# Optimization experiments

Hardware: AMD Instinct MI355X
Metric: run time of the kernel (lower is better)

The kernel has to match this reference:

```python
import jax, jax.numpy as jnp
import numpy as np

SHIFTS = 1
WINDOW_SIZES = (4, 8, 16)
BN_EPS = 1e-5


def _calc_attn_path(x, ws, shifts):
    # x: (b, H, W, 2c) with channels laid out as (qv=2, c)
    b, H, W, c2 = x.shape
    c = c2 // 2
    if shifts > 0:
        x = jnp.roll(x, shift=(-ws // 2, -ws // 2), axis=(1, 2))
    h, w = H // ws, W // ws
    # 'b (h dh) (w dw) (qv c) -> qv (b h w) (dh dw c)'
    qv = x.reshape(b, h, ws, w, ws, 2, c).transpose(5, 0, 1, 3, 2, 4, 6)
    qv = qv.reshape(2, b * h * w, ws * ws * c)
    q, v = qv[0], qv[1]                       # (N, D), N = b*h*w windows, D = ws*ws*c
    atn = jax.nn.softmax(q @ q.T, axis=-1)    # (N, N) attention across windows (as in source)
    y = atn @ v                               # (N, D)
    # '(b h w) (dh dw c) -> b (h dh) (w dw) c'
    y = y.reshape(b, h, w, ws, ws, c).transpose(0, 1, 3, 2, 4, 5).reshape(b, H, W, c)
    if shifts > 0:
        y = jnp.roll(y, shift=(ws // 2, ws // 2), axis=(1, 2))
    return y, atn


def setup_inputs() -> dict:
    key = jax.random.key(0)
    ks = jax.random.split(key, 3)
    B, H, W, C = 4, 128, 128, 180
    inputs = jax.random.normal(ks[0], (B, H, W, C), jnp.float32)
    conv1_w = jax.random.normal(ks[1], (1, 1, C, 2 * C), jnp.float32) * 0.05
    conv1_b = jnp.zeros((2 * C,), jnp.float32)
    bn_scale = jnp.ones((2 * C,), jnp.float32)
    bn_bias = jnp.zeros((2 * C,), jnp.float32)
    conv2_w = jax.random.normal(ks[2], (1, 1, C, C), jnp.float32) * 0.05
    conv2_b = jnp.zeros((C,), jnp.float32)
    return {"inputs": inputs, "conv1_w": conv1_w, "conv1_b": conv1_b,
            "bn_scale": bn_scale, "bn_bias": bn_bias,
            "conv2_w": conv2_w, "conv2_b": conv2_b}


def reference(inputs, conv1_w, conv1_b, bn_scale, bn_bias, conv2_w, conv2_b):
    # 1x1 conv to 2*C channels (calc_attn=True)
    x = jnp.einsum('bhwc,cd->bhwd', inputs, conv1_w[0, 0]) + conv1_b
    # BatchNorm in training mode (batch statistics)
    mean = x.mean(axis=(0, 1, 2))
    var = x.var(axis=(0, 1, 2))
    x = (x - mean) * jax.lax.rsqrt(var + BN_EPS) * bn_scale + bn_bias
    xs = jnp.split(x, 3, axis=-1)             # three groups of 2*C/3 channels
    ys, attns = [], []
    for ws, xi in zip(WINDOW_SIZES, xs):
        y, a = _calc_attn_path(xi, ws, SHIFTS)
        ys.append(y)
        attns.append(a)
    y = jnp.concatenate(ys, axis=-1)          # back to C channels
    y = jnp.einsum('bhwc,cd->bhwd', y, conv2_w[0, 0]) + conv2_b
    return (y, *attns)
```

## Files before the change

### kernel.cpp

```cpp
#include <hip/hip_runtime.h>

typedef unsigned short u16;
typedef __bf16 bf16x8 __attribute__((ext_vector_type(8)));
typedef float f32x4 __attribute__((ext_vector_type(4)));
typedef u16 u16x4 __attribute__((ext_vector_type(4)));
typedef u16 u16x8 __attribute__((ext_vector_type(8)));

__device__ __forceinline__ u16 f2bf(float v) {
    unsigned u = __float_as_uint(v);
    unsigned r = (u + 0x7fffu + ((u >> 16) & 1u)) >> 16;
    return (u16)r;
}
__device__ __forceinline__ float bf2f(u16 u) { return __uint_as_float(((unsigned)u) << 16); }

__device__ __forceinline__ void async_cp16(const u16* g, u16* l) {
    __builtin_amdgcn_global_load_lds((const __attribute__((address_space(1))) unsigned int*)g,
                                     (__attribute__((address_space(3))) unsigned int*)l, 16, 0, 0);
}

__device__ __forceinline__ int xcd_swz(int local, int n) {
    const int q = n >> 3, r = n & 7;
    const int xcd = local & 7, j = local >> 3;
    const int base = xcd < r ? xcd * (q + 1) : r * (q + 1) + (xcd - r) * q;
    return base + j;
}

#define LKSWZ(tid) ((((tid) & 3) ^ (((tid) >> 3) & 3)) << 3)
#define ROSWZ(lane) (((lane) & 15) * 32 + ((((lane) >> 4) ^ (((lane) >> 1) & 3)) << 3))

__global__ __launch_bounds__(256) void gemm_f32(
    const u16* __restrict__ A, const u16* __restrict__ B,
    float* __restrict__ C, const float* __restrict__ bias,
    int K, int ldc, int n_store)
{
    __shared__ char smem[32768];
    u16* As = (u16*)smem;
    u16* Bs = (u16*)(smem + 8192);
    const int tid = threadIdx.x;
    const int lane = tid & 63;
    const int wave = tid >> 6;
    const int wm = wave >> 1, wn = wave & 1;
    const long m0 = (long)blockIdx.y * 128;
    const long n0 = (long)blockIdx.x * 128;

    f32x4 acc[4][4] = {};
    const int lrow = tid >> 2;
    const int lk = LKSWZ(tid);
    const u16* Ag = A + (m0 + lrow) * (long)K + lk;
    const u16* Bg = B + (n0 + lrow) * (long)K + lk;
    u16* Asl = As + tid * 8;
    u16* Bsl = Bs + tid * 8;
    const long K64 = (long)64 * K;
    const int ro = ROSWZ(lane);
    const int nsteps = K >> 5;

    async_cp16(Ag, Asl);
    async_cp16(Ag + K64, Asl + 2048);
    async_cp16(Bg, Bsl);
    async_cp16(Bg + K64, Bsl + 2048);
    __syncthreads();

    int cur = 0;
    for (int s = 0; s < nsteps; s++) {
        if (s + 1 < nsteps) {
            const int kn = (s + 1) << 5;
            u16* An = Asl + ((cur ^ 1) << 13);
            u16* Bn = Bsl + ((cur ^ 1) << 13);
            async_cp16(Ag + kn, An);
            async_cp16(Ag + kn + K64, An + 2048);
            async_cp16(Bg + kn, Bn);
            async_cp16(Bg + kn + K64, Bn + 2048);
        }
        bf16x8 af[4], bg[4];
        const u16* Asc = As + (cur << 13);
        const u16* Bsc = Bs + (cur << 13);
#pragma unroll
        for (int i = 0; i < 4; i++) af[i] = *(const bf16x8*)(Asc + (wm * 64 + i * 16) * 32 + ro);
#pragma unroll
        for (int j = 0; j < 4; j++) bg[j] = *(const bf16x8*)(Bsc + (wn * 64 + j * 16) * 32 + ro);
#pragma unroll
        for (int i = 0; i < 4; i++)
#pragma unroll
            for (int j = 0; j < 4; j++)
                acc[i][j] = __builtin_amdgcn_mfma_f32_16x16x32_bf16(af[i], bg[j], acc[i][j], 0, 0, 0);
        __syncthreads();
        cur ^= 1;
    }

    float bv[4];
#pragma unroll
    for (int j = 0; j < 4; j++) bv[j] = bias[n0 + wn * 64 + j * 16 + (lane & 15)];

    float* Cs = (float*)smem;
    for (int c = 0; c < 4; c++) {
        __syncthreads();
        if (wm == (c >> 1)) {
#pragma unroll
            for (int ii = 0; ii < 2; ii++) {
                const int i = (c & 1) * 2 + ii;
#pragma unroll
                for (int j = 0; j < 4; j++)
#pragma unroll
                    for (int r = 0; r < 4; r++) {
                        const int lr = ii * 16 + ((lane >> 4) << 2) + r;
                        Cs[lr * 128 + wn * 64 + j * 16 + (lane & 15)] = acc[i][j][r] + bv[j];
                    }
            }
        }
        __syncthreads();
        const int lr = tid >> 3;
        const int cg = (tid & 7) * 16;
        const long rowg = m0 + c * 32 + lr;
#pragma unroll
        for (int e = 0; e < 4; e++) {
            const int colg = cg + e * 4;
            if ((int)n0 + colg < n_store)
                *(f32x4*)(C + rowg * (long)ldc + n0 + colg) = *(const f32x4*)(Cs + lr * 128 + colg);
        }
    }
}

__global__ __launch_bounds__(256) void conv1_gemm(
    const float* __restrict__ A, const u16* __restrict__ B,
    u16* __restrict__ C, const float* __restrict__ bias)
{
    __shared__ char smem[16384];
    u16* As = (u16*)smem;
    u16* Bs = (u16*)(smem + 8192);
    const int tid = threadIdx.x;
    const int lane = tid & 63;
    const int wave = tid >> 6;
    const int wm = wave >> 1, wn = wave & 1;
    const long m0 = (long)blockIdx.y * 128;
    const long n0 = (long)blockIdx.x * 128;

    f32x4 acc[4][4] = {};
    const int lrow = tid >> 2;
    const int lk = LKSWZ(tid);
    const float* Ar0 = A + (m0 + lrow) * 180L;
    const float* Ar1 = Ar0 + 64 * 180L;
    const u16* Bg = B + (n0 + lrow) * 192L + lk;
    u16* Asl = As + tid * 8;
    u16* Bsl = Bs + tid * 8;
    const int ro = ROSWZ(lane);

#pragma unroll
    for (int k0 = 0; k0 < 192; k0 += 32) {
        const int gk = k0 + lk;
        u16x8 oa, ob;
        if (gk + 8 <= 180) {
            f32x4 a0 = *(const f32x4*)(Ar0 + gk), a1 = *(const f32x4*)(Ar0 + gk + 4);
            f32x4 b0 = *(const f32x4*)(Ar1 + gk), b1 = *(const f32x4*)(Ar1 + gk + 4);
#pragma unroll
            for (int c = 0; c < 4; c++) {
                oa[c] = f2bf(a0[c]); oa[4 + c] = f2bf(a1[c]);
                ob[c] = f2bf(b0[c]); ob[4 + c] = f2bf(b1[c]);
            }
        } else if (gk < 180) {
            f32x4 a0 = *(const f32x4*)(Ar0 + gk);
            f32x4 b0 = *(const f32x4*)(Ar1 + gk);
#pragma unroll
            for (int c = 0; c < 4; c++) {
                oa[c] = f2bf(a0[c]); oa[4 + c] = 0;
                ob[c] = f2bf(b0[c]); ob[4 + c] = 0;
            }
        } else {
#pragma unroll
            for (int c = 0; c < 8; c++) { oa[c] = 0; ob[c] = 0; }
        }
        *(u16x8*)Asl = oa;
        *(u16x8*)(Asl + 2048) = ob;
        async_cp16(Bg + k0, Bsl);
        async_cp16(Bg + k0 + 64 * 192, Bsl + 2048);
        __syncthreads();
        bf16x8 af[4], bg[4];
#pragma unroll
        for (int i = 0; i < 4; i++) af[i] = *(const bf16x8*)(As + (wm * 64 + i * 16) * 32 + ro);
#pragma unroll
        for (int j = 0; j < 4; j++) bg[j] = *(const bf16x8*)(Bs + (wn * 64 + j * 16) * 32 + ro);
#pragma unroll
        for (int i = 0; i < 4; i++)
#pragma unroll
            for (int j = 0; j < 4; j++)
                acc[i][j] = __builtin_amdgcn_mfma_f32_16x16x32_bf16(af[i], bg[j], acc[i][j], 0, 0, 0);
        __syncthreads();
    }

    float bv[4];
#pragma unroll
    for (int j = 0; j < 4; j++) bv[j] = bias[n0 + wn * 64 + j * 16 + (lane & 15)];

    u16* Cs = (u16*)smem;
    for (int c = 0; c < 2; c++) {
        __syncthreads();
        if (wm == c) {
#pragma unroll
            for (int i = 0; i < 4; i++)
#pragma unroll
                for (int j = 0; j < 4; j++)
#pragma unroll
                    for (int r = 0; r < 4; r++) {
                        const int lr = i * 16 + ((lane >> 4) << 2) + r;
                        Cs[lr * 128 + wn * 64 + j * 16 + (lane & 15)] = f2bf(acc[i][j][r] + bv[j]);
                    }
        }
        __syncthreads();
        const int lr = tid >> 2;
        const int cg = (tid & 3) * 32;
        const long rowg = m0 + c * 64 + lr;
#pragma unroll
        for (int e = 0; e < 4; e++) {
            const int colg = cg + e * 8;
            *(u16x8*)(C + rowg * 384L + n0 + colg) = *(const u16x8*)(Cs + lr * 128 + colg);
        }
    }
}

#define KLOOP_3BUF(Asv, Bsv, Aslv, Bslv, AgV, BgV, kbegV, K64V, nstepsV, roV)                 \
    {                                                                                          \
        async_cp16(AgV + kbegV, Aslv);                                                         \
        async_cp16(AgV + kbegV + K64V, Aslv + 2048);                                           \
        async_cp16(BgV + kbegV, Bslv);                                                         \
        async_cp16(BgV + kbegV + K64V, Bslv + 2048);                                           \
        if (nstepsV > 1) {                                                                     \
            const int kn = kbegV + 32;                                                         \
            async_cp16(AgV + kn, Aslv + 8192);                                                 \
            async_cp16(AgV + kn + K64V, Aslv + 8192 + 2048);                                   \
            async_cp16(BgV + kn, Bslv + 8192);                                                 \
            async_cp16(BgV + kn + K64V, Bslv + 8192 + 2048);                                   \
        }                                                                                      \
        int rb = 0, wb = 2;                                                                    \
        for (int s = 0; s < nstepsV; s++) {                                                    \
            if (s + 1 < nstepsV) { asm volatile("s_waitcnt vmcnt(4)" ::: "memory"); }          \
            else                 { asm volatile("s_waitcnt vmcnt(0)" ::: "memory"); }          \
            __builtin_amdgcn_sched_barrier(0);                                                 \
            __builtin_amdgcn_s_barrier();                                                      \
            __builtin_amdgcn_sched_barrier(0);                                                 \
            if (s + 2 < nstepsV) {                                                             \
                const int kn = kbegV + ((s + 2) << 5);                                         \
                u16* An = Aslv + wb * 8192;                                                    \
                u16* Bn = Bslv + wb * 8192;                                                    \
                async_cp16(AgV + kn, An);                                                      \
                async_cp16(AgV + kn + K64V, An + 2048);                                        \
                async_cp16(BgV + kn, Bn);                                                      \
                async_cp16(BgV + kn + K64V, Bn + 2048);                                        \
            }                                                                                  \
            bf16x8 af[4], bgf[4];                                                              \
            const u16* Asc = Asv + rb * 8192;                                                  \
            const u16* Bsc = Bsv + rb * 8192;                                                  \
            _Pragma("unroll")                                                                  \
            for (int i = 0; i < 4; i++) af[i] = *(const bf16x8*)(Asc + (wm * 64 + i * 16) * 32 + roV); \
            _Pragma("unroll")                                                                  \
            for (int j = 0; j < 4; j++) bgf[j] = *(const bf16x8*)(Bsc + (wn * 64 + j * 16) * 32 + roV); \
            _Pragma("unroll")                                                                  \
            for (int i = 0; i < 4; i++)                                                        \
                _Pragma("unroll")                                                              \
                for (int j = 0; j < 4; j++)                                                    \
                    acc[i][j] = __builtin_amdgcn_mfma_f32_16x16x32_bf16(af[i], bgf[j], acc[i][j], 0, 0, 0); \
            rb = rb == 2 ? 0 : rb + 1;                                                         \
            wb = wb == 2 ? 0 : wb + 1;                                                         \
        }                                                                                      \
    }

__global__ __launch_bounds__(256, 3) void qq_all(
    const u16* __restrict__ q0, const u16* __restrict__ q1, const u16* __restrict__ q2,
    float* __restrict__ S0, float* __restrict__ pG1, float* __restrict__ pG2)
{
    __shared__ char smem[49152];
    u16* As = (u16*)smem;
    u16* Bs = (u16*)(smem + 8192);
    const int bid = blockIdx.x;
    int seg, local;
    if (bid < 528) { seg = 0; local = xcd_swz(bid, 528); }
    else if (bid < 816) { seg = 1; local = xcd_swz(bid - 528, 288); }
    else { seg = 2; local = xcd_swz(bid - 816, 180); }
    const int tX = seg == 0 ? 32 : (seg == 1 ? 8 : 2);
    const int TT = (tX * (tX + 1)) >> 1;
    const int K = seg == 0 ? 1024 : (seg == 1 ? 3840 : 15360);
    const int Ksplit = seg == 0 ? 1024 : (seg == 1 ? 480 : 256);
    const int N = seg == 0 ? 4096 : (seg == 1 ? 1024 : 256);
    const u16* A = seg == 0 ? q0 : (seg == 1 ? q1 : q2);
    float* outP = seg == 0 ? S0 : (seg == 1 ? pG1 : pG2);
    const int z = local / TT;
    int rem = local - z * TT;
    int by = 0, rowlen = tX;
    while (rem >= rowlen) { rem -= rowlen; by++; rowlen--; }
    const int bx = by + rem;

    const int tid = threadIdx.x;
    const int lane = tid & 63;
    const int wave = tid >> 6;
    const int wm = wave >> 1, wn = wave & 1;
    const long m0 = (long)by * 128;
    const long n0 = (long)bx * 128;
    const int kbeg = z * Ksplit;

    f32x4 acc[4][4] = {};
    const int lrow = tid >> 2;
    const int lk = LKSWZ(tid);
    const u16* Ag = A + (m0 + lrow) * (long)K + lk;
    const u16* Bg = A + (n0 + lrow) * (long)K + lk;
    u16* Asl = As + tid * 8;
    u16* Bsl = Bs + tid * 8;
    const long K64 = (long)64 * K;
    const int ro = ROSWZ(lane);
    const int nsteps = Ksplit >> 5;

    KLOOP_3BUF(As, Bs, Asl, Bsl, Ag, Bg, kbeg, K64, nsteps, ro);

    float* Pz = outP + (long)z * N * N;

    if (bx != by) {
        const int r0 = (int)n0 + wn * 64 + (lane & 15);
        const int c0 = (int)m0 + wm * 64 + ((lane >> 4) << 2);
#pragma unroll
        for (int j = 0; j < 4; j++) {
            float* rp = Pz + (long)(r0 + j * 16) * N + c0;
#pragma unroll
            for (int i = 0; i < 4; i++)
                *(f32x4*)(rp + i * 16) = acc[i][j];
        }
    }

    float* Cs = (float*)smem;
    for (int c = 0; c < 4; c++) {
        __syncthreads();
        if (wm == (c >> 1)) {
#pragma unroll
            for (int ii = 0; ii < 2; ii++) {
                const int i = (c & 1) * 2 + ii;
#pragma unroll
                for (int j = 0; j < 4; j++)
#pragma unroll
                    for (int r = 0; r < 4; r++) {
                        const int lr = ii * 16 + ((lane >> 4) << 2) + r;
                        Cs[lr * 128 + wn * 64 + j * 16 + (lane & 15)] = acc[i][j][r];
                    }
            }
        }
        __syncthreads();
        const int lr = tid >> 3;
        const int cg = (tid & 7) * 16;
        const long rowg = m0 + c * 32 + lr;
#pragma unroll
        for (int e = 0; e < 4; e++) {
            const int colg = cg + e * 4;
            *(f32x4*)(Pz + rowg * (long)N + n0 + colg) = *(const f32x4*)(Cs + lr * 128 + colg);
        }
    }
}

__global__ __launch_bounds__(256, 3) void pv_all(
    const u16* __restrict__ a0, const u16* __restrict__ a1, const u16* __restrict__ a2,
    const u16* __restrict__ vt0, const u16* __restrict__ vt1, const u16* __restrict__ vt2,
    u16* __restrict__ Ysp, float* __restrict__ pP0, float* __restrict__ pP1)
{
    __shared__ char smem[49152];
    u16* As = (u16*)smem;
    u16* Bs = (u16*)(smem + 8192);
    const int bid = blockIdx.x;
    int seg, local, z = 0;
    if (bid < 512) { seg = 0; const int l = xcd_swz(bid, 512); z = l >> 8; local = l & 255; }
    else if (bid < 752) { seg = 1; local = xcd_swz(bid - 512, 240); }
    else { seg = 2; local = xcd_swz(bid - 752, 240); }
    const int tX = seg == 0 ? 8 : (seg == 1 ? 30 : 120);
    const int K = seg == 0 ? 4096 : (seg == 1 ? 1024 : 256);
    const int Ksplit = seg == 0 ? 2048 : K;
    const int D = seg == 0 ? 960 : (seg == 1 ? 3840 : 15360);
    const int l2ws = 2 + seg;
    const int l2wc = 5 - seg;
    const u16* A = seg == 0 ? a0 : (seg == 1 ? a1 : a2);
    const u16* B = seg == 0 ? vt0 : (seg == 1 ? vt1 : vt2);
    const int bx = local % tX;
    const int by = local / tX;

    const int tid = threadIdx.x;
    const int lane = tid & 63;
    const int wave = tid >> 6;
    const int wm = wave >> 1, wn = wave & 1;
    const long m0 = (long)by * 128;
    const long n0 = (long)bx * 128;
    const int kbeg = z * Ksplit;

    f32x4 acc[4][4] = {};
    const int lrow = tid >> 2;
    const int lk = LKSWZ(tid);
    const u16* Ag = A + (m0 + lrow) * (long)K + lk;
    const u16* Bg = B + (n0 + lrow) * (long)K + lk;
    u16* Asl = As + tid * 8;
    u16* Bsl = Bs + tid * 8;
    const long K64 = (long)64 * K;
    const int ro = ROSWZ(lane);
    const int nsteps = Ksplit >> 5;

    KLOOP_3BUF(As, Bs, Asl, Bsl, Ag, Bg, kbeg, K64, nsteps, ro);

    if (seg == 0) {
        float* Pz = (z == 0) ? pP0 : pP1;
        float* Cs = (float*)smem;
        for (int c = 0; c < 4; c++) {
            __syncthreads();
            if (wm == (c >> 1)) {
#pragma unroll
                for (int ii = 0; ii < 2; ii++) {
                    const int i = (c & 1) * 2 + ii;
#pragma unroll
                    for (int j = 0; j < 4; j++)
#pragma unroll
                        for (int r = 0; r < 4; r++) {
                            const int lr = ii * 16 + ((lane >> 4) << 2) + r;
                            Cs[lr * 128 + wn * 64 + j * 16 + (lane & 15)] = acc[i][j][r];
                        }
                }
            }
            __syncthreads();
            const int lr = tid >> 3;
            const int cg = (tid & 7) * 16;
            const long rowg = m0 + c * 32 + lr;
#pragma unroll
            for (int e = 0; e < 4; e++) {
                const int colg = cg + e * 4;
                *(f32x4*)(Pz + rowg * 1024L + n0 + colg) = *(const f32x4*)(Cs + lr * 128 + colg);
            }
        }
        return;
    }

    u16* Cs = (u16*)smem;
    const int wcm = (1 << l2wc) - 1;
    const int wsm = (1 << l2ws) - 1;
    const int sh = 1 << (l2ws - 1);
    for (int c = 0; c < 2; c++) {
        __syncthreads();
        if (wm == c) {
#pragma unroll
            for (int i = 0; i < 4; i++)
#pragma unroll
                for (int j = 0; j < 4; j++)
#pragma unroll
                    for (int r = 0; r < 4; r++) {
                        const int lr = i * 16 + ((lane >> 4) << 2) + r;
                        Cs[lr * 128 + wn * 64 + j * 16 + (lane & 15)] = f2bf(acc[i][j][r]);
                    }
        }
        __syncthreads();
        const int lr = tid >> 2;
        const int cgbase = (tid & 3) * 32;
        const int n = (int)m0 + c * 64 + lr;
        const int wi = n & wcm;
        const int hi = (n >> l2wc) & wcm;
        const int bb = n >> (2 * l2wc);
        const int rowb = (hi << l2ws) + sh;
        const int colb = (wi << l2ws) + sh;
        const long bbase = (long)bb * 128 * 128 * 192 + 60 * seg;
#pragma unroll
        for (int e = 0; e < 8; e++) {
            const int colg = cgbase + e * 4;
            const int d = (int)n0 + colg;
            if (d < D) {
                const int cc = d % 60;
                const int pp = d / 60;
                const int dh = pp >> l2ws;
                const int dw = pp & wsm;
                const int row = (rowb + dh) & 127;
                const int col = (colb + dw) & 127;
                *(u16x4*)(Ysp + bbase + ((long)row * 128 + col) * 192 + cc) =
                    *(const u16x4*)(Cs + lr * 128 + colg);
            }
        }
    }
}

__global__ __launch_bounds__(256) void reduce_scatter_g0(
    const float* __restrict__ pP0, const float* __restrict__ pP1, u16* __restrict__ Ysp)
{
    const int n = blockIdx.x;
    const int d = threadIdx.x * 4;
    if (d >= 960) return;
    const long i = (long)n * 1024 + d;
    f32x4 s = *(const f32x4*)(pP0 + i) + *(const f32x4*)(pP1 + i);
    const int cc = d % 60;
    const int pp = d / 60;
    const int dh = pp >> 2;
    const int dw = pp & 3;
    const int wi = n & 31;
    const int hi = (n >> 5) & 31;
    const int b = n >> 10;
    const int row = ((hi << 2) + dh + 2) & 127;
    const int col = ((wi << 2) + dw + 2) & 127;
    u16x4 o;
#pragma unroll
    for (int c = 0; c < 4; c++) o[c] = f2bf(s[c]);
    *(u16x4*)(Ysp + ((long)((b << 7) + row) * 128 + col) * 192 + cc) = o;
}

__global__ __launch_bounds__(256) void zero_pad(u16* __restrict__ Ysp)
{
    const long r = (long)blockIdx.x * 256 + threadIdx.x;
    u16* p = Ysp + r * 192 + 180;
    const u16x4 z = {0, 0, 0, 0};
    *(u16x4*)(p) = z;
    *(u16x4*)(p + 4) = z;
    *(u16x4*)(p + 8) = z;
}

__global__ __launch_bounds__(192) void prep_all(
    const float* __restrict__ W1, const float* __restrict__ W2,
    const float* __restrict__ b1, const float* __restrict__ b2,
    u16* __restrict__ W1t, u16* __restrict__ W2t,
    float* __restrict__ b1p, float* __restrict__ b2p, float* __restrict__ accum)
{
    const int bid = blockIdx.x;
    const int t = threadIdx.x;
    if (bid < 384) {
        W1t[bid * 192 + t] = (bid < 360 && t < 180) ? f2bf(W1[t * 360 + bid]) : (u16)0;
    } else if (bid < 640) {
        const int n = bid - 384;
        W2t[n * 192 + t] = (n < 180 && t < 180) ? f2bf(W2[t * 180 + n]) : (u16)0;
    } else {
#pragma unroll
        for (int j = 0; j < 4; j++) {
            const int i = t + 192 * j;
            if (i < 384) b1p[i] = (i < 360) ? b1[i] : 0.0f;
            else if (i < 640) { const int k = i - 384; b2p[k] = (k < 180) ? b2[k] : 0.0f; }
            if (i < 768) accum[i] = 0.0f;
        }
    }
}

__global__ __launch_bounds__(384) void bn_stats(const u16* __restrict__ x, float* __restrict__ accum)
{
    const int ch = threadIdx.x;
    const long base = (long)blockIdx.x * 256 * 384;
    float s = 0.0f, s2 = 0.0f;
    for (int r = 0; r < 256; r++) {
        const float v = bf2f(x[base + (long)r * 384 + ch]);
        s += v; s2 += v * v;
    }
    atomicAdd(&accum[ch], s);
    atomicAdd(&accum[384 + ch], s2);
}

__global__ __launch_bounds__(256) void gather_all(
    const u16* __restrict__ x, const float* __restrict__ accum,
    const float* __restrict__ bns, const float* __restrict__ bnb,
    u16* __restrict__ q0, u16* __restrict__ q1, u16* __restrict__ q2,
    u16* __restrict__ vt0, u16* __restrict__ vt1, u16* __restrict__ vt2)
{
    __shared__ u16 t[64][65];
    const int bid = blockIdx.x;
    int seg, local;
    if (bid < 1024) { seg = 0; local = bid; }
    else if (bid < 1984) { seg = 1; local = bid - 1024; }
    else { seg = 2; local = bid - 1984; }
    const int tX = seg == 0 ? 16 : (seg == 1 ? 60 : 240);
    const int N = seg == 0 ? 4096 : (seg == 1 ? 1024 : 256);
    const int D = seg == 0 ? 960 : (seg == 1 ? 3840 : 15360);
    const int Dp = seg == 0 ? 1024 : (seg == 1 ? 3840 : 15360);
    const int l2ws = 2 + seg;
    const int l2wc = 5 - seg;
    u16* q = seg == 0 ? q0 : (seg == 1 ? q1 : q2);
    u16* vt = seg == 0 ? vt0 : (seg == 1 ? vt1 : vt2);
    const int bx = local % tX;
    const int by = local / tX;

    const int d0 = bx * 64;
    const int n0 = by * 64;
    const int tc = threadIdx.x & 63;
    const int tr = threadIdx.x >> 6;

    const int d = d0 + tc;
    const int sh = 1 << (l2ws - 1);
    const int cc = d % 60;
    const int pp = d / 60;
    const int dh = pp >> l2ws;
    const int dw = pp & ((1 << l2ws) - 1);
    const int wcm = (1 << l2wc) - 1;
    const int ch = 120 * seg + cc;
    const float m_q = accum[ch] * (1.0f / 65536.0f);
    const float v_q = accum[384 + ch] * (1.0f / 65536.0f) - m_q * m_q;
    const float seq = bns[ch] * rsqrtf(v_q + 1e-5f);
    const float beq = bnb[ch] - m_q * seq;
    const float m_v = accum[ch + 60] * (1.0f / 65536.0f);
    const float v_v = accum[384 + ch + 60] * (1.0f / 65536.0f) - m_v * m_v;
    const float sev = bns[ch + 60] * rsqrtf(v_v + 1e-5f);
    const float bev = bnb[ch + 60] - m_v * sev;
    const bool valid = d < D;

#pragma unroll 4
    for (int i = 0; i < 16; i++) {
        const int n = n0 + i * 4 + tr;
        const int wi = n & wcm;
        const int hi = (n >> l2wc) & wcm;
        const int b = n >> (2 * l2wc);
        const int row = ((hi << l2ws) + dh + sh) & 127;
        const int col = ((wi << l2ws) + dw + sh) & 127;
        const long src = ((long)((b << 7) + row) * 128 + col) * 384 + ch;
        const float xq = bf2f(x[src]);
        const float xv = bf2f(x[src + 60]);
        q[(long)n * Dp + d] = valid ? f2bf(seq * xq + beq) : (u16)0;
        t[tc][i * 4 + tr] = f2bf(sev * xv + bev);
    }
    __syncthreads();
#pragma unroll 4
    for (int i = 0; i < 16; i++) {
        const int dd = i * 4 + tr;
        vt[(long)(d0 + dd) * N + n0 + tc] = t[dd][tc];
    }
}

template <int VPT>
__device__ __forceinline__ void softmax_body(
    const float* __restrict__ P, int nsplit, long MN, int rowi,
    float* __restrict__ S, u16* __restrict__ Sb)
{
    const int N = VPT * 256;
    const long base = (long)rowi * N;
    float v[VPT];
    float mx = -3.0e38f;
#pragma unroll
    for (int i = 0; i < VPT; i++) {
        const long idx = base + i * 256 + threadIdx.x;
        float val = P[idx];
        for (int z = 1; z < nsplit; z++) val += P[(long)z * MN + idx];
        v[i] = val; mx = fmaxf(mx, val);
    }
#pragma unroll
    for (int o = 32; o > 0; o >>= 1) mx = fmaxf(mx, __shfl_down(mx, o, 64));
    __shared__ float redm[4];
    if ((threadIdx.x & 63) == 0) redm[threadIdx.x >> 6] = mx;
    __syncthreads();
    mx = fmaxf(fmaxf(redm[0], redm[1]), fmaxf(redm[2], redm[3]));
    float s = 0.0f;
#pragma unroll
    for (int i = 0; i < VPT; i++) { v[i] = __expf(v[i] - mx); s += v[i]; }
#pragma unroll
    for (int o = 32; o > 0; o >>= 1) s += __shfl_down(s, o, 64);
    __shared__ float reds[4];
    if ((threadIdx.x & 63) == 0) reds[threadIdx.x >> 6] = s;
    __syncthreads();
    s = reds[0] + reds[1] + reds[2] + reds[3];
    const float inv = 1.0f / s;
#pragma unroll
    for (int i = 0; i < VPT; i++) {
        const float r = v[i] * inv;
        const long idx = base + i * 256 + threadIdx.x;
        S[idx] = r;
        Sb[idx] = f2bf(r);
    }
}

__global__ __launch_bounds__(256) void softmax_all(
    float* __restrict__ S0, const float* __restrict__ pG1, const float* __restrict__ pG2,
    float* __restrict__ out1, float* __restrict__ out2,
    u16* __restrict__ ab0, u16* __restrict__ ab1, u16* __restrict__ ab2)
{
    const int r = blockIdx.x;
    if (r < 4096)      softmax_body<16>(S0, 1, 16777216L, r, S0, ab0);
    else if (r < 5120) softmax_body<4>(pG1, 8, 1048576L, r - 4096, out1, ab1);
    else               softmax_body<1>(pG2, 60, 65536L, r - 5120, out2, ab2);
}

extern "C" void kernel_launch(void* const* d_in, const int* in_sizes, int n_in,
                              void* d_out, int out_size, void* d_ws, size_t ws_size,
                              hipStream_t stream)
{
    const float* in_x = (const float*)d_in[0];
    const float* w1  = (const float*)d_in[1];
    const float* b1  = (const float*)d_in[2];
    const float* bns = (const float*)d_in[3];
    const float* bnb = (const float*)d_in[4];
    const float* w2  = (const float*)d_in[5];
    const float* b2  = (const float*)d_in[6];
    float* out = (float*)d_out;

    char* w = (char*)d_ws;
    u16* atnb0 = (u16*)w;
    size_t off = 33554432;
    u16* x = (u16*)(w + off);
    float* pG1 = (float*)(w + off);
    float* pG2 = (float*)(w + off + 33554432);
    u16* Ysp = (u16*)(w + off);
    float* pP1 = (float*)(w + off + 25165824);
    off += 50331648;
    u16* W1t = (u16*)(w + off);  off += 147456;
    u16* W2t = (u16*)(w + off);  off += 98304;
    float* b1p = (float*)(w + off);   off += 4096;
    float* b2p = (float*)(w + off);   off += 4096;
    float* accum = (float*)(w + off); off += 4096;
    u16* q0 = (u16*)(w + off);  off += 8388608;
    u16* q1 = (u16*)(w + off);  off += 7864320;
    u16* q2 = (u16*)(w + off);  off += 7864320;
    u16* vt0 = (u16*)(w + off); off += 8388608;
    u16* vt1 = (u16*)(w + off); off += 7864320;
    u16* vt2 = (u16*)(w + off); off += 7864320;
    u16* atnb1 = (u16*)(w + off); off += 2097152;
    u16* atnb2 = (u16*)(w + off); off += 131072;
    float* pP0 = (float*)q0;

    float* S0 = out + 11796480L;
    float* S1 = out + 28573696L;
    float* S2 = out + 29622272L;

    prep_all<<<641, 192, 0, stream>>>(w1, w2, b1, b2, W1t, W2t, b1p, b2p, accum);
    conv1_gemm<<<dim3(3, 512), 256, 0, stream>>>(in_x, W1t, x, b1p);
    bn_stats<<<256, 384, 0, stream>>>(x, accum);
    gather_all<<<2944, 256, 0, stream>>>(x, accum, bns, bnb, q0, q1, q2, vt0, vt1, vt2);
    qq_all<<<996, 256, 0, stream>>>(q0, q1, q2, S0, pG1, pG2);
    softmax_all<<<5376, 256, 0, stream>>>(S0, pG1, pG2, S1, S2, atnb0, atnb1, atnb2);
    zero_pad<<<256, 256, 0, stream>>>(Ysp);
    pv_all<<<992, 256, 0, stream>>>(atnb0, atnb1, atnb2, vt0, vt1, vt2, Ysp, pP0, pP1);
    reduce_scatter_g0<<<4096, 256, 0, stream>>>(pP0, pP1, Ysp);
    gemm_f32<<<dim3(2, 512), 256, 0, stream>>>(Ysp, W2t, out, b2p, 192, 180, 180);
}
```

Measured before the change: 428.2 us.

## Load A operand fragments directly from global into registers, stage only B in LDS

The qq_all and pv_all K-loops no longer stage the A tile through shared memory. Each wave loads its own A fragments straight from global memory into registers, double-buffered two steps ahead, while B keeps the triple-buffered async LDS path. LDS drops from 48KB to 24KB per block, and the LDS reads and traffic for A go away. In exchange, the two waves that share a row band each fetch the same A rows from global (wider reads that rely on cache), register pressure rises under the 3-blocks-per-SM bound, and the wait counts now depend on mixed vmcnt ordering.

```diff
diff --git a/kernel.cpp b/kernel.cpp
--- a/kernel.cpp
+++ b/kernel.cpp
@@ -18,6 +18,12 @@
                                      (__attribute__((address_space(3))) unsigned int*)l, 16, 0, 0);
 }
 
+__device__ __forceinline__ bf16x8 gload16(const u16* g) {
+    f32x4 t;
+    asm volatile("global_load_dwordx4 %0, %1, off" : "=v"(t) : "v"(g) : "memory");
+    return __builtin_bit_cast(bf16x8, t);
+}
+
 __device__ __forceinline__ int xcd_swz(int local, int n) {
     const int q = n >> 3, r = n & 7;
     const int xcd = local & 7, j = local >> 3;
@@ -27,6 +33,58 @@
 
 #define LKSWZ(tid) ((((tid) & 3) ^ (((tid) >> 3) & 3)) << 3)
 #define ROSWZ(lane) (((lane) & 15) * 32 + ((((lane) >> 4) ^ (((lane) >> 1) & 3)) << 3))
+
+#define BBUF 4096
+
+#define KSTEP(AC, s_)                                                                         \
+    {                                                                                          \
+        if ((s_) + 1 < nsteps) { asm volatile("s_waitcnt vmcnt(6)" ::: "memory"); }            \
+        else                   { asm volatile("s_waitcnt vmcnt(0)" ::: "memory"); }            \
+        __builtin_amdgcn_sched_barrier(0);                                                     \
+        __builtin_amdgcn_s_barrier();                                                          \
+        __builtin_amdgcn_sched_barrier(0);                                                     \
+        if ((s_) + 2 < nsteps) {                                                               \
+            const int kn = kbeg + (((s_) + 2) << 5);                                           \
+            u16* Bn = Bsl + wb * BBUF;                                                         \
+            async_cp16(Bg + kn, Bn);                                                           \
+            async_cp16(Bg + kn + K64, Bn + 2048);                                              \
+        }                                                                                      \
+        const u16* Bsc = Bs + rb * BBUF;                                                       \
+        bf16x8 bfr[4];                                                                         \
+        _Pragma("unroll")                                                                      \
+        for (int j = 0; j < 4; j++) bfr[j] = *(const bf16x8*)(Bsc + (wn * 64 + j * 16) * 32 + ro); \
+        _Pragma("unroll")                                                                      \
+        for (int i = 0; i < 4; i++)                                                            \
+            _Pragma("unroll")                                                                  \
+            for (int j = 0; j < 4; j++)                                                        \
+                acc[i][j] = __builtin_amdgcn_mfma_f32_16x16x32_bf16(AC[i], bfr[j], acc[i][j], 0, 0, 0); \
+        if ((s_) + 2 < nsteps) {                                                               \
+            const int kf = (((s_) + 2) << 5);                                                  \
+            _Pragma("unroll")                                                                  \
+            for (int i = 0; i < 4; i++) AC[i] = gload16(Af[i] + kf);                           \
+        }                                                                                      \
+        rb = rb == 2 ? 0 : rb + 1;                                                             \
+        wb = wb == 2 ? 0 : wb + 1;                                                             \
+    }
+
+#define KLOOP_AREG()                                                                           \
+    {                                                                                          \
+        async_cp16(Bg + kbeg, Bsl);                                                            \
+        async_cp16(Bg + kbeg + K64, Bsl + 2048);                                               \
+        _Pragma("unroll")                                                                      \
+        for (int i = 0; i < 4; i++) a0[i] = gload16(Af[i]);                                    \
+        if (nsteps > 1) {                                                                      \
+            async_cp16(Bg + kbeg + 32, Bsl + BBUF);                                            \
+            async_cp16(Bg + kbeg + 32 + K64, Bsl + BBUF + 2048);                               \
+            _Pragma("unroll")                                                                  \
+            for (int i = 0; i < 4; i++) a1[i] = gload16(Af[i] + 32);                           \
+        }                                                                                      \
+        int rb = 0, wb = 2;                                                                    \
+        for (int s = 0; s < nsteps; s += 2) {                                                  \
+            KSTEP(a0, s);                                                                      \
+            if (s + 1 < nsteps) KSTEP(a1, s + 1);                                              \
+        }                                                                                      \
+    }
 
 __global__ __launch_bounds__(256) void gemm_f32(
     const u16* __restrict__ A, const u16* __restrict__ B,
@@ -216,59 +274,12 @@
     }
 }
 
-#define KLOOP_3BUF(Asv, Bsv, Aslv, Bslv, AgV, BgV, kbegV, K64V, nstepsV, roV)                 \
-    {                                                                                          \
-        async_cp16(AgV + kbegV, Aslv);                                                         \
-        async_cp16(AgV + kbegV + K64V, Aslv + 2048);                                           \
-        async_cp16(BgV + kbegV, Bslv);                                                         \
-        async_cp16(BgV + kbegV + K64V, Bslv + 2048);                                           \
-        if (nstepsV > 1) {                                                                     \
-            const int kn = kbegV + 32;                                                         \
-            async_cp16(AgV + kn, Aslv + 8192);                                                 \
-            async_cp16(AgV + kn + K64V, Aslv + 8192 + 2048);                                   \
-            async_cp16(BgV + kn, Bslv + 8192);                                                 \
-            async_cp16(BgV + kn + K64V, Bslv + 8192 + 2048);                                   \
-        }                                                                                      \
-        int rb = 0, wb = 2;                                                                    \
-        for (int s = 0; s < nstepsV; s++) {                                                    \
-            if (s + 1 < nstepsV) { asm volatile("s_waitcnt vmcnt(4)" ::: "memory"); }          \
-            else                 { asm volatile("s_waitcnt vmcnt(0)" ::: "memory"); }          \
-            __builtin_amdgcn_sched_barrier(0);                                                 \
-            __builtin_amdgcn_s_barrier();                                                      \
-            __builtin_amdgcn_sched_barrier(0);                                                 \
-            if (s + 2 < nstepsV) {                                                             \
-                const int kn = kbegV + ((s + 2) << 5);                                         \
-                u16* An = Aslv + wb * 8192;                                                    \
-                u16* Bn = Bslv + wb * 8192;                                                    \
-                async_cp16(AgV + kn, An);                                                      \
-                async_cp16(AgV + kn + K64V, An + 2048);                                        \
-                async_cp16(BgV + kn, Bn);                                                      \
-                async_cp16(BgV + kn + K64V, Bn + 2048);                                        \
-            }                                                                                  \
-            bf16x8 af[4], bgf[4];                                                              \
-            const u16* Asc = Asv + rb * 8192;                                                  \
-            const u16* Bsc = Bsv + rb * 8192;                                                  \
-            _Pragma("unroll")                                                                  \
-            for (int i = 0; i < 4; i++) af[i] = *(const bf16x8*)(Asc + (wm * 64 + i * 16) * 32 + roV); \
-            _Pragma("unroll")                                                                  \
-            for (int j = 0; j < 4; j++) bgf[j] = *(const bf16x8*)(Bsc + (wn * 64 + j * 16) * 32 + roV); \
-            _Pragma("unroll")                                                                  \
-            for (int i = 0; i < 4; i++)                                                        \
-                _Pragma("unroll")                                                              \
-                for (int j = 0; j < 4; j++)                                                    \
-                    acc[i][j] = __builtin_amdgcn_mfma_f32_16x16x32_bf16(af[i], bgf[j], acc[i][j], 0, 0, 0); \
-            rb = rb == 2 ? 0 : rb + 1;                                                         \
-            wb = wb == 2 ? 0 : wb + 1;                                                         \
-        }                                                                                      \
-    }
-
 __global__ __launch_bounds__(256, 3) void qq_all(
     const u16* __restrict__ q0, const u16* __restrict__ q1, const u16* __restrict__ q2,
     float* __restrict__ S0, float* __restrict__ pG1, float* __restrict__ pG2)
 {
-    __shared__ char smem[49152];
-    u16* As = (u16*)smem;
-    u16* Bs = (u16*)(smem + 8192);
+    __shared__ char smem[24576];
+    u16* Bs = (u16*)smem;
     const int bid = blockIdx.x;
     int seg, local;
     if (bid < 528) { seg = 0; local = xcd_swz(bid, 528); }
@@ -298,15 +309,19 @@
     f32x4 acc[4][4] = {};
     const int lrow = tid >> 2;
     const int lk = LKSWZ(tid);
-    const u16* Ag = A + (m0 + lrow) * (long)K + lk;
     const u16* Bg = A + (n0 + lrow) * (long)K + lk;
-    u16* Asl = As + tid * 8;
     u16* Bsl = Bs + tid * 8;
     const long K64 = (long)64 * K;
     const int ro = ROSWZ(lane);
     const int nsteps = Ksplit >> 5;
 
-    KLOOP_3BUF(As, Bs, Asl, Bsl, Ag, Bg, kbeg, K64, nsteps, ro);
+    const u16* Af[4];
+#pragma unroll
+    for (int i = 0; i < 4; i++)
+        Af[i] = A + (m0 + wm * 64 + i * 16 + (lane & 15)) * (long)K + kbeg + ((lane >> 4) << 3);
+
+    bf16x8 a0[4], a1[4];
+    KLOOP_AREG();
 
     float* Pz = outP + (long)z * N * N;
 
@@ -351,13 +366,12 @@
 }
 
 __global__ __launch_bounds__(256, 3) void pv_all(
-    const u16* __restrict__ a0, const u16* __restrict__ a1, const u16* __restrict__ a2,
+    const u16* __restrict__ a0p, const u16* __restrict__ a1p, const u16* __restrict__ a2p,
     const u16* __restrict__ vt0, const u16* __restrict__ vt1, const u16* __restrict__ vt2,
     u16* __restrict__ Ysp, float* __restrict__ pP0, float* __restrict__ pP1)
 {
-    __shared__ char smem[49152];
-    u16* As = (u16*)smem;
-    u16* Bs = (u16*)(smem + 8192);
+    __shared__ char smem[24576];
+    u16* Bs = (u16*)smem;
     const int bid = blockIdx.x;
     int seg, local, z = 0;
     if (bid < 512) { seg = 0; const int l = xcd_swz(bid, 512); z = l >> 8; local = l & 255; }
@@ -369,7 +383,7 @@
     const int D = seg == 0 ? 960 : (seg == 1 ? 3840 : 15360);
     const int l2ws = 2 + seg;
     const int l2wc = 5 - seg;
-    const u16* A = seg == 0 ? a0 : (seg == 1 ? a1 : a2);
+    const u16* A = seg == 0 ? a0p : (seg == 1 ? a1p : a2p);
     const u16* B = seg == 0 ? vt0 : (seg == 1 ? vt1 : vt2);
     const int bx = local % tX;
     const int by = local / tX;
@@ -385,15 +399,19 @@
     f32x4 acc[4][4] = {};
     const int lrow = tid >> 2;
     const int lk = LKSWZ(tid);
-    const u16* Ag = A + (m0 + lrow) * (long)K + lk;
     const u16* Bg = B + (n0 + lrow) * (long)K + lk;
-    u16* Asl = As + tid * 8;
     u16* Bsl = Bs + tid * 8;
     const long K64 = (long)64 * K;
     const int ro = ROSWZ(lane);
     const int nsteps = Ksplit >> 5;
 
-    KLOOP_3BUF(As, Bs, Asl, Bsl, Ag, Bg, kbeg, K64, nsteps, ro);
+    const u16* Af[4];
+#pragma unroll
+    for (int i = 0; i < 4; i++)
+        Af[i] = A + (m0 + wm * 64 + i * 16 + (lane & 15)) * (long)K + kbeg + ((lane >> 4) << 3);
+
+    bf16x8 a0[4], a1[4];
+    KLOOP_AREG();
 
     if (seg == 0) {
         float* Pz = (z == 0) ? pP0 : pP1;
```

After: 495.2 us. 1.16x slower.
